# Kernel optimization log

Measured on AMD Instinct MI355X. Metric: run time of the kernel, lower is better.

The kernel has to match this reference:

```python
import jax, jax.numpy as jnp
import numpy as np

N, E = 50000, 1600000
D_IN, D_HID, D_OUT = 256, 256, 128  # 2*output_dim = 256, output_dim = 128


def glorot(key, shape):
    fan_in, fan_out = shape
    limit = np.sqrt(6.0 / (fan_in + fan_out)).astype(np.float32)
    return jax.random.uniform(key, shape, jnp.float32, -limit, limit)


def setup_inputs() -> dict:
    key = jax.random.key(0)
    k0, k1, k2, k3 = jax.random.split(key, 4)
    x = jax.random.normal(k0, (N, D_IN), jnp.float32)
    edge_index = jax.random.randint(k1, (2, E), 0, N, jnp.int32)
    W1 = glorot(k2, (D_IN, D_HID))
    b1 = jnp.zeros((D_HID,), jnp.float32)
    W2 = glorot(k3, (D_HID, D_OUT))
    b2 = jnp.zeros((D_OUT,), jnp.float32)
    return {"x": x, "edge_index": edge_index, "W1": W1, "b1": b1, "W2": W2, "b2": b2}


def gcn_propagate(x, src, dst, num_nodes):
    """One hop of D^-1/2 (A + I) D^-1/2 @ x (PyG gcn_norm with self-loops)."""
    loops = jnp.arange(num_nodes, dtype=src.dtype)
    src_sl = jnp.concatenate([src, loops])  # [E + N]
    dst_sl = jnp.concatenate([dst, loops])
    ones = jnp.ones(src_sl.shape, x.dtype)
    deg = jax.ops.segment_sum(ones, dst_sl, num_segments=num_nodes)  # >= 1 (self-loop)
    dinv = jax.lax.rsqrt(jnp.maximum(deg, 1e-12))
    norm = dinv[src_sl] * dinv[dst_sl]  # [E + N]
    msgs = x[src_sl] * norm[:, None]    # gather + scale, [E+N, D]
    return jax.ops.segment_sum(msgs, dst_sl, num_segments=num_nodes)


def reference(x, edge_index, W1, b1, W2, b2):
    src, dst = edge_index[0], edge_index[1]
    n = x.shape[0]
    # SGConv(K=1): propagate then linear. conv1 + ReLU
    h = jax.nn.relu(gcn_propagate(x, src, dst, n) @ W1 + b1)
    # conv2 (GAE branch)
    return gcn_propagate(h, src, dst, n) @ W2 + b2
```

## Files before the change

### kernel.cpp

```cpp
#include <hip/hip_runtime.h>

typedef short s16x8 __attribute__((ext_vector_type(8)));
typedef float f32x4 __attribute__((ext_vector_type(4)));
typedef float f32x2 __attribute__((ext_vector_type(2)));

#define TILE 2048

__device__ __forceinline__ unsigned int brne(float f) {
    unsigned int u = __float_as_uint(f);
    return (u + 0x7FFFu + ((u >> 16) & 1u)) >> 16;
}
__device__ __forceinline__ float blo(unsigned int u) { return __uint_as_float(u << 16); }
__device__ __forceinline__ float bhi(unsigned int u) { return __uint_as_float(u & 0xFFFF0000u); }

__device__ __forceinline__ unsigned int pk_bf16(float lo, float hi) {
    unsigned int r;
    asm("v_cvt_pk_bf16_f32 %0, %1, %2" : "=v"(r) : "v"(lo), "v"(hi));
    return r;
}

__device__ __forceinline__ void acc8p(f32x2* a, const uint4 u, const f32x2 w2) {
    a[0] += (f32x2){blo(u.x), bhi(u.x)} * w2;
    a[1] += (f32x2){blo(u.y), bhi(u.y)} * w2;
    a[2] += (f32x2){blo(u.z), bhi(u.z)} * w2;
    a[3] += (f32x2){blo(u.w), bhi(u.w)} * w2;
}

__device__ __forceinline__ void acc16p(f32x2* a, const uint4 u, const f32x2 w2) {
    a[0] += __builtin_amdgcn_cvt_pk_f32_fp8((int)u.x, false) * w2;
    a[1] += __builtin_amdgcn_cvt_pk_f32_fp8((int)u.x, true)  * w2;
    a[2] += __builtin_amdgcn_cvt_pk_f32_fp8((int)u.y, false) * w2;
    a[3] += __builtin_amdgcn_cvt_pk_f32_fp8((int)u.y, true)  * w2;
    a[4] += __builtin_amdgcn_cvt_pk_f32_fp8((int)u.z, false) * w2;
    a[5] += __builtin_amdgcn_cvt_pk_f32_fp8((int)u.z, true)  * w2;
    a[6] += __builtin_amdgcn_cvt_pk_f32_fp8((int)u.w, false) * w2;
    a[7] += __builtin_amdgcn_cvt_pk_f32_fp8((int)u.w, true)  * w2;
}


__global__ void k_bhist(const int* __restrict__ dst, int* __restrict__ bucket_cnt,
                        int e, int nb) {
    __shared__ int h[256];
    const int tid = threadIdx.x;
    h[tid] = 0;
    __syncthreads();
    const int base = blockIdx.x * TILE + tid;
#pragma unroll
    for (int k = 0; k < 8; k++) {
        const int i = base + k * 256;
        if (i < e) atomicAdd(&h[dst[i] >> 8], 1);
    }
    __syncthreads();
    if (tid < nb && h[tid]) atomicAdd(&bucket_cnt[tid], h[tid]);
}

__global__ void k_bscatter(const int* __restrict__ src, const int* __restrict__ dst,
                           const int* __restrict__ bcnt, int* __restrict__ bbase,
                           int* __restrict__ bcur, uint2* __restrict__ eb, int e, int nb) {
    __shared__ int sh[256], sbase[256], h[256], hbase[256], h2[256];
    const int tid = threadIdx.x;
    const int v = (tid < nb) ? bcnt[tid] : 0;
    int x = v;
    sh[tid] = x;
    __syncthreads();
    for (int off = 1; off < 256; off <<= 1) {
        const int t = (tid >= off) ? sh[tid - off] : 0;
        __syncthreads();
        if (tid >= off) { x += t; sh[tid] = x; }
        __syncthreads();
    }
    sbase[tid] = x - v;
    if (blockIdx.x == 0) {
        if (tid < nb) bbase[tid] = x - v;
        if (tid == 0) bbase[nb] = e;
    }
    h[tid] = 0; h2[tid] = 0;
    __syncthreads();
    const int base = blockIdx.x * TILE + tid;
    int s[8], d[8], b[8];
    bool val[8];
#pragma unroll
    for (int k = 0; k < 8; k++) {
        const int i = base + k * 256;
        val[k] = i < e;
        if (val[k]) {
            s[k] = src[i]; d[k] = dst[i]; b[k] = d[k] >> 8;
            atomicAdd(&h[b[k]], 1);
        }
    }
    __syncthreads();
    if (h[tid]) hbase[tid] = sbase[tid] + atomicAdd(&bcur[tid], h[tid]);
    __syncthreads();
#pragma unroll
    for (int k = 0; k < 8; k++) {
        if (val[k]) {
            const int off = atomicAdd(&h2[b[k]], 1);
            eb[hbase[b[k]] + off] = make_uint2((unsigned)s[k], (unsigned)d[k]);
        }
    }
}

__global__ void k_nhist_scan(const uint2* __restrict__ eb, const int* __restrict__ bucket_base,
                             int* __restrict__ rowptr, int* __restrict__ part,
                             float* __restrict__ dinv, int n) {
    __shared__ int c[256], sh[256];
    const int tid = threadIdx.x, b = blockIdx.x;
    c[tid] = 0;
    __syncthreads();
    const int beg = bucket_base[b], end = bucket_base[b + 1];
    for (int i = beg + tid; i < end; i += 256)
        atomicAdd(&c[eb[i].y & 255], 1);
    __syncthreads();
    const int v = c[tid];
    const int node = b * 256 + tid;
    if (node < n) dinv[node] = rsqrtf((float)(v + 1));
    int x = v;
    sh[tid] = x;
    __syncthreads();
    for (int off = 1; off < 256; off <<= 1) {
        const int t = (tid >= off) ? sh[tid - off] : 0;
        __syncthreads();
        if (tid >= off) { x += t; sh[tid] = x; }
        __syncthreads();
    }
    if (node <= n) rowptr[node] = x - v;
    if (tid == 255) part[b] = x;
}

template <bool PREW>
__global__ void k_place(const uint2* __restrict__ eb, const int* __restrict__ bucket_base,
                        int* __restrict__ rowptr, const int* __restrict__ part,
                        void* __restrict__ esv, const float* __restrict__ dinv,
                        int n, int nb) {
    __shared__ int sh[256], rp[256], offs[256];
    __shared__ float sdv[256];
    const int tid = threadIdx.x, b = blockIdx.x;
    int x = (tid < nb) ? part[tid] : 0;
    sh[tid] = x;
    __syncthreads();
    for (int off = 1; off < 256; off <<= 1) {
        const int t = (tid >= off) ? sh[tid - off] : 0;
        __syncthreads();
        if (tid >= off) { x += t; sh[tid] = x; }
        __syncthreads();
    }
    const int prefix = (b > 0) ? sh[b - 1] : 0;
    const int node = b * 256 + tid;
    int rg = 0;
    if (node <= n) {
        rg = rowptr[node] + prefix;
        rowptr[node] = rg;
    }
    rp[tid] = rg;
    offs[tid] = 0;
    if (PREW) sdv[tid] = (node < n) ? dinv[node] : 0.f;
    __syncthreads();
    const int beg = bucket_base[b], end = bucket_base[b + 1];
    if (PREW) {
        int2* es2 = (int2*)esv;
        for (int i = beg + tid; i < end; i += 256) {
            const uint2 ed = eb[i];
            const int sI = (int)ed.x, d = (int)ed.y & 255;
            const float w = dinv[sI] * sdv[d];
            const int local = atomicAdd(&offs[d], 1);
            es2[rp[d] + local] = make_int2(sI, __float_as_int(w));
        }
    } else {
        int* es1 = (int*)esv;
        for (int i = beg + tid; i < end; i += 256) {
            const uint2 ed = eb[i];
            const int d = (int)ed.y & 255;
            const int local = atomicAdd(&offs[d], 1);
            es1[rp[d] + local] = (int)ed.x;
        }
    }
}

__global__ void k_tW2(const float* __restrict__ W1, const float* __restrict__ W2,
                      unsigned short* __restrict__ W1t, unsigned short* __restrict__ W2t) {
    const int t = blockIdx.x * 256 + threadIdx.x;
    if (t < 65536) {
        const int k = t >> 8, nn = t & 255;
        W1t[nn * 256 + k] = (unsigned short)brne(W1[t]);
    } else {
        const int u = t - 65536;
        const int k = u >> 7, nn = u & 127;
        W2t[nn * 256 + k] = (unsigned short)brne(W2[u]);
    }
}

#define LP 40
template <bool AF32, bool FP8OUT>
__global__ __launch_bounds__(256) void k_gemm(const void* __restrict__ Av,
                                              const unsigned short* __restrict__ Bt,
                                              void* __restrict__ Cout,
                                              int M, int Nc) {
    __shared__ unsigned short As[2][128 * LP];
    __shared__ unsigned short Bs[2][128 * LP];

    const int tid = threadIdx.x;
    const int wave = tid >> 6, lane = tid & 63;
    const int wm = (wave >> 1) * 64, wn = (wave & 1) * 64;
    const int l15 = lane & 15, quad = lane >> 4;
    const int mBase = blockIdx.x * 128, nBase = blockIdx.y * 128;

    f32x4 acc[4][4];
#pragma unroll
    for (int i = 0; i < 4; i++)
#pragma unroll
        for (int j = 0; j < 4; j++) acc[i][j] = (f32x4){0.f, 0.f, 0.f, 0.f};

    const int r0 = tid >> 2, kc0 = tid & 3;
    int am0 = mBase + r0;      if (am0 >= M) am0 = M - 1;
    int am1 = mBase + r0 + 64; if (am1 >= M) am1 = M - 1;

    const uint4* Ap0; const uint4* Ap1; const float4* Af0; const float4* Af1;
    if (AF32) {
        Af0 = (const float4*)Av + (size_t)am0 * 64 + kc0 * 2;
        Af1 = (const float4*)Av + (size_t)am1 * 64 + kc0 * 2;
    } else {
        Ap0 = (const uint4*)Av + (size_t)am0 * 32 + kc0;
        Ap1 = (const uint4*)Av + (size_t)am1 * 32 + kc0;
    }
    const uint4* Bp0 = (const uint4*)Bt + (size_t)(nBase + r0) * 32 + kc0;
    const uint4* Bp1 = (const uint4*)Bt + (size_t)(nBase + r0 + 64) * 32 + kc0;

    uint4 a0, a1, b0, b1;
    auto LOAD = [&](int kt) {
        if (AF32) {
            const float4 l0 = Af0[kt * 8], h0 = Af0[kt * 8 + 1];
            const float4 l1 = Af1[kt * 8], h1 = Af1[kt * 8 + 1];
            a0.x = pk_bf16(l0.x, l0.y); a0.y = pk_bf16(l0.z, l0.w);
            a0.z = pk_bf16(h0.x, h0.y); a0.w = pk_bf16(h0.z, h0.w);
            a1.x = pk_bf16(l1.x, l1.y); a1.y = pk_bf16(l1.z, l1.w);
            a1.z = pk_bf16(h1.x, h1.y); a1.w = pk_bf16(h1.z, h1.w);
        } else {
            a0 = Ap0[kt * 4];
            a1 = Ap1[kt * 4];
        }
        b0 = Bp0[kt * 4];
        b1 = Bp1[kt * 4];
    };
    auto STORE = [&](int buf) {
        *(uint4*)&As[buf][r0 * LP + kc0 * 8] = a0;
        *(uint4*)&As[buf][(r0 + 64) * LP + kc0 * 8] = a1;
        *(uint4*)&Bs[buf][r0 * LP + kc0 * 8] = b0;
        *(uint4*)&Bs[buf][(r0 + 64) * LP + kc0 * 8] = b1;
    };

    LOAD(0);
    STORE(0);
    __syncthreads();
    for (int kt = 0; kt < 8; ++kt) {
        const int cur = kt & 1;
        if (kt < 7) LOAD(kt + 1);
        s16x8 af[4], bf[4];
#pragma unroll
        for (int i = 0; i < 4; i++)
            af[i] = *(const s16x8*)&As[cur][(wm + i * 16 + l15) * LP + quad * 8];
#pragma unroll
        for (int j = 0; j < 4; j++)
            bf[j] = *(const s16x8*)&Bs[cur][(wn + j * 16 + l15) * LP + quad * 8];
        if (kt < 7) STORE(cur ^ 1);
#pragma unroll
        for (int i = 0; i < 4; i++)
#pragma unroll
            for (int j = 0; j < 4; j++)
                acc[i][j] = __builtin_amdgcn_mfma_f32_16x16x32_bf16(af[i], bf[j], acc[i][j], 0, 0, 0);
        __syncthreads();
    }

#pragma unroll
    for (int i = 0; i < 4; i++) {
        const int rowb = mBase + wm + i * 16 + quad * 4;
#pragma unroll
        for (int j = 0; j < 4; j++) {
            const int col = nBase + wn + j * 16 + l15;
#pragma unroll
            for (int r = 0; r < 4; r += 2) {
                if (FP8OUT) {
                    const unsigned int pk = __builtin_amdgcn_cvt_pk_fp8_f32(
                        acc[i][j][r], acc[i][j][r + 1], 0, false);
                    if (rowb + r < M)
                        ((unsigned char*)Cout)[(size_t)(rowb + r) * Nc + col] =
                            (unsigned char)pk;
                    if (rowb + r + 1 < M)
                        ((unsigned char*)Cout)[(size_t)(rowb + r + 1) * Nc + col] =
                            (unsigned char)(pk >> 8);
                } else {
                    const unsigned int pk = pk_bf16(acc[i][j][r], acc[i][j][r + 1]);
                    if (rowb + r < M)
                        ((unsigned short*)Cout)[(size_t)(rowb + r) * Nc + col] =
                            (unsigned short)pk;
                    if (rowb + r + 1 < M)
                        ((unsigned short*)Cout)[(size_t)(rowb + r + 1) * Nc + col] =
                            (unsigned short)(pk >> 16);
                }
            }
        }
    }
}


template <bool PREW>
__global__ void k_prop256f8(const uint4* __restrict__ X4,
                            const int* __restrict__ rowptr,
                            const void* __restrict__ esv,
                            const float* __restrict__ dinv,
                            const float* __restrict__ bias,
                            uint4* __restrict__ Y4, int n) {
    const int wid = (int)((blockIdx.x * blockDim.x + threadIdx.x) >> 6);
    const int lane = threadIdx.x & 63;
    const int quad = lane >> 4, l16 = lane & 15;
    if (wid >= n) return;
    const float dd = dinv[wid];
    const int2* es2 = (const int2*)esv;
    const int*  es1 = (const int*)esv;
    f32x2 a[8];
#pragma unroll
    for (int k = 0; k < 8; k++) a[k] = (f32x2){0.f, 0.f};

    const int beg = rowptr[wid], end = rowptr[wid + 1];
    int j = beg + quad;

    auto EDGE = [&](int jj, int& s, float& w) {
        const bool v = jj < end;
        const int idx = v ? jj : 0;
        if (PREW) {
            const int2 p = es2[idx];
            s = p.x;
            w = v ? __int_as_float(p.y) : 0.f;
        } else {
            s = es1[idx];
            w = v ? dinv[s] * dd : 0.f;
        }
    };

    int s0, s1, s2, s3;
    float w0, w1, w2, w3;
    EDGE(j, s0, w0); EDGE(j + 4, s1, w1); EDGE(j + 8, s2, w2); EDGE(j + 12, s3, w3);

    if (quad == 0) {
        const uint4 v = X4[(size_t)wid * 16 + l16];
        acc16p(a, v, (f32x2){dd * dd, dd * dd});
    }

    while (j + 12 < end) {
        const uint4 u0 = X4[(size_t)s0 * 16 + l16];
        const uint4 u1 = X4[(size_t)s1 * 16 + l16];
        const uint4 u2 = X4[(size_t)s2 * 16 + l16];
        const uint4 u3 = X4[(size_t)s3 * 16 + l16];
        j += 16;
        int t0, t1, t2, t3;
        float x0, x1, x2, x3;
        EDGE(j, t0, x0); EDGE(j + 4, t1, x1); EDGE(j + 8, t2, x2); EDGE(j + 12, t3, x3);
        acc16p(a, u0, (f32x2){w0, w0});
        acc16p(a, u1, (f32x2){w1, w1});
        acc16p(a, u2, (f32x2){w2, w2});
        acc16p(a, u3, (f32x2){w3, w3});
        s0 = t0; s1 = t1; s2 = t2; s3 = t3;
        w0 = x0; w1 = x1; w2 = x2; w3 = x3;
    }
    {
        const uint4 u0 = X4[(size_t)s0 * 16 + l16];
        const uint4 u1 = X4[(size_t)s1 * 16 + l16];
        const uint4 u2 = X4[(size_t)s2 * 16 + l16];
        acc16p(a, u0, (f32x2){w0, w0});
        acc16p(a, u1, (f32x2){w1, w1});
        acc16p(a, u2, (f32x2){w2, w2});
    }
#pragma unroll
    for (int k = 0; k < 8; k++) {
        a[k][0] += __shfl_xor(a[k][0], 16);
        a[k][1] += __shfl_xor(a[k][1], 16);
        a[k][0] += __shfl_xor(a[k][0], 32);
        a[k][1] += __shfl_xor(a[k][1], 32);
    }
    if (quad == 0) {
        const float4* bp = (const float4*)bias + l16 * 4;
#pragma unroll
        for (int q = 0; q < 4; q++) {
            const float4 b = bp[q];
            a[2 * q][0]     = fmaxf(a[2 * q][0] + b.x, 0.f);
            a[2 * q][1]     = fmaxf(a[2 * q][1] + b.y, 0.f);
            a[2 * q + 1][0] = fmaxf(a[2 * q + 1][0] + b.z, 0.f);
            a[2 * q + 1][1] = fmaxf(a[2 * q + 1][1] + b.w, 0.f);
        }
        uint4 p0, p1;
        p0.x = pk_bf16(a[0][0], a[0][1]);
        p0.y = pk_bf16(a[1][0], a[1][1]);
        p0.z = pk_bf16(a[2][0], a[2][1]);
        p0.w = pk_bf16(a[3][0], a[3][1]);
        p1.x = pk_bf16(a[4][0], a[4][1]);
        p1.y = pk_bf16(a[5][0], a[5][1]);
        p1.z = pk_bf16(a[6][0], a[6][1]);
        p1.w = pk_bf16(a[7][0], a[7][1]);
        Y4[(size_t)wid * 32 + l16 * 2] = p0;
        Y4[(size_t)wid * 32 + l16 * 2 + 1] = p1;
    }
}

template <bool PREW>
__global__ void k_prop128b(const uint4* __restrict__ X4,
                           const int* __restrict__ rowptr,
                           const void* __restrict__ esv,
                           const float* __restrict__ dinv,
                           const float* __restrict__ bias,
                           float* __restrict__ Yout, int n) {
    const int wid = (int)((blockIdx.x * blockDim.x + threadIdx.x) >> 6);
    const int lane = threadIdx.x & 63;
    const int quad = lane >> 4, l16 = lane & 15;
    if (wid >= n) return;
    const float dd = dinv[wid];
    const int2* es2 = (const int2*)esv;
    const int*  es1 = (const int*)esv;
    f32x2 a[4];
#pragma unroll
    for (int k = 0; k < 4; k++) a[k] = (f32x2){0.f, 0.f};

    const int beg = rowptr[wid], end = rowptr[wid + 1];
    int j = beg + quad;

    auto EDGE = [&](int jj, int& s, float& w) {
        const bool v = jj < end;
        const int idx = v ? jj : 0;
        if (PREW) {
            const int2 p = es2[idx];
            s = p.x;
            w = v ? __int_as_float(p.y) : 0.f;
        } else {
            s = es1[idx];
            w = v ? dinv[s] * dd : 0.f;
        }
    };

    int s0, s1, s2, s3;
    float w0, w1, w2, w3;
    EDGE(j, s0, w0); EDGE(j + 4, s1, w1); EDGE(j + 8, s2, w2); EDGE(j + 12, s3, w3);

    if (quad == 0) {
        const uint4 v = X4[(size_t)wid * 16 + l16];
        acc8p(a, v, (f32x2){dd * dd, dd * dd});
    }

    while (j + 12 < end) {
        const uint4 u0 = X4[(size_t)s0 * 16 + l16];
        const uint4 u1 = X4[(size_t)s1 * 16 + l16];
        const uint4 u2 = X4[(size_t)s2 * 16 + l16];
        const uint4 u3 = X4[(size_t)s3 * 16 + l16];
        j += 16;
        int t0, t1, t2, t3;
        float x0, x1, x2, x3;
        EDGE(j, t0, x0); EDGE(j + 4, t1, x1); EDGE(j + 8, t2, x2); EDGE(j + 12, t3, x3);
        acc8p(a, u0, (f32x2){w0, w0});
        acc8p(a, u1, (f32x2){w1, w1});
        acc8p(a, u2, (f32x2){w2, w2});
        acc8p(a, u3, (f32x2){w3, w3});
        s0 = t0; s1 = t1; s2 = t2; s3 = t3;
        w0 = x0; w1 = x1; w2 = x2; w3 = x3;
    }
    {
        const uint4 u0 = X4[(size_t)s0 * 16 + l16];
        const uint4 u1 = X4[(size_t)s1 * 16 + l16];
        const uint4 u2 = X4[(size_t)s2 * 16 + l16];
        acc8p(a, u0, (f32x2){w0, w0});
        acc8p(a, u1, (f32x2){w1, w1});
        acc8p(a, u2, (f32x2){w2, w2});
    }
#pragma unroll
    for (int k = 0; k < 4; k++) {
        a[k][0] += __shfl_xor(a[k][0], 16);
        a[k][1] += __shfl_xor(a[k][1], 16);
        a[k][0] += __shfl_xor(a[k][0], 32);
        a[k][1] += __shfl_xor(a[k][1], 32);
    }
    if (quad == 0) {
        const float4 b0 = ((const float4*)bias)[l16 * 2];
        const float4 b1 = ((const float4*)bias)[l16 * 2 + 1];
        float4* op = (float4*)Yout + (size_t)wid * 32 + l16 * 2;
        op[0] = make_float4(a[0][0] + b0.x, a[0][1] + b0.y, a[1][0] + b0.z, a[1][1] + b0.w);
        op[1] = make_float4(a[2][0] + b1.x, a[2][1] + b1.y, a[3][0] + b1.z, a[3][1] + b1.w);
    }
}

extern "C" void kernel_launch(void* const* d_in, const int* in_sizes, int n_in,
                              void* d_out, int out_size, void* d_ws, size_t ws_size,
                              hipStream_t stream) {
    const float* x  = (const float*)d_in[0];
    const int*   ei = (const int*)d_in[1];
    const float* W1 = (const float*)d_in[2];
    const float* b1 = (const float*)d_in[3];
    const float* W2 = (const float*)d_in[4];
    const float* b2 = (const float*)d_in[5];
    float* out = (float*)d_out;

    const int n = in_sizes[0] / 256;
    const int e = in_sizes[1] / 2;
    const int* src = ei;
    const int* dst = ei + e;
    const int nb = (n + 255) >> 8;

    auto al = [](size_t v) { return (v + 511) & ~(size_t)511; };
    const size_t fixed = al(sizeof(float) * n) + al(sizeof(int) * (n + 1)) +
                         al(1024) + al(2048) + al(sizeof(int) * 257) +
                         al(2ull * 256 * 256) + al(2ull * 128 * 256) +
                         al((size_t)n * 256) + al(2ull * n * 256) + al(2ull * n * 128);
    const bool prew = (fixed + al(8ull * (size_t)e)) <= ws_size;

    char* wsp = (char*)d_ws;
    size_t off = 0;
    auto alloc = [&](size_t bytes) -> char* {
        char* p = wsp + off;
        off += (bytes + 511) & ~(size_t)511;
        return p;
    };
    float* dinv    = (float*)alloc(sizeof(float) * n);
    int*   rowptr  = (int*)alloc(sizeof(int) * (n + 1));
    int*   part    = (int*)alloc(1024);
    int*   bcc     = (int*)alloc(2048);
    int*   bcnt    = bcc;
    int*   bcur    = bcc + 256;
    int*   bbase   = (int*)alloc(sizeof(int) * 257);
    void*  es      = (void*)alloc((prew ? 8ull : 4ull) * (size_t)e);
    unsigned short* W1t = (unsigned short*)alloc(2ull * 256 * 256);
    unsigned short* W2t = (unsigned short*)alloc(2ull * 128 * 256);
    unsigned char*  T1  = (unsigned char*)alloc((size_t)n * 256);
    unsigned short* H   = (unsigned short*)alloc(2ull * n * 256);
    unsigned short* T2  = (unsigned short*)alloc(2ull * n * 128);
    uint2* eb = (uint2*)H;

    const int nb_t = (e + TILE - 1) / TILE;

    static hipStream_t sB = nullptr;
    static hipEvent_t evF = nullptr, evW = nullptr;
    static int inited = 0;
    if (!inited) {
        inited = 1;
        if (hipStreamCreateWithFlags(&sB, hipStreamNonBlocking) != hipSuccess) sB = nullptr;
        if (hipEventCreateWithFlags(&evF, hipEventDisableTiming) != hipSuccess) evF = nullptr;
        if (hipEventCreateWithFlags(&evW, hipEventDisableTiming) != hipSuccess) evW = nullptr;
    }
    const bool par = (sB != nullptr) && (evF != nullptr) && (evW != nullptr);
    hipStream_t gs = par ? sB : stream;

    if (par) {
        (void)hipEventRecord(evF, stream);
        (void)hipStreamWaitEvent(sB, evF, 0);
    }

    k_tW2<<<(65536 + 32768) / 256, 256, 0, gs>>>(W1, W2, W1t, W2t);
    dim3 g1((n + 127) / 128, 2);
    k_gemm<true, true><<<g1, 256, 0, gs>>>(x, W1t, T1, n, 256);
    if (par) (void)hipEventRecord(evW, gs);

    (void)hipMemsetAsync(bcc, 0, 2048, stream);
    k_bhist<<<nb_t, 256, 0, stream>>>(dst, bcnt, e, nb);
    k_bscatter<<<nb_t, 256, 0, stream>>>(src, dst, bcnt, bbase, bcur, eb, e, nb);
    k_nhist_scan<<<nb, 256, 0, stream>>>(eb, bbase, rowptr, part, dinv, n);
    if (prew)
        k_place<true><<<nb, 256, 0, stream>>>(eb, bbase, rowptr, part, es, dinv, n, nb);
    else
        k_place<false><<<nb, 256, 0, stream>>>(eb, bbase, rowptr, part, es, dinv, n, nb);

    if (par) (void)hipStreamWaitEvent(stream, evW, 0);

    if (prew)
        k_prop256f8<true><<<(n + 3) / 4, 256, 0, stream>>>((const uint4*)T1, rowptr, es,
                                                           dinv, b1, (uint4*)H, n);
    else
        k_prop256f8<false><<<(n + 3) / 4, 256, 0, stream>>>((const uint4*)T1, rowptr, es,
                                                            dinv, b1, (uint4*)H, n);

    dim3 g2((n + 127) / 128, 1);
    k_gemm<false, false><<<g2, 256, 0, stream>>>(H, W2t, T2, n, 128);
    if (prew)
        k_prop128b<true><<<(n + 3) / 4, 256, 0, stream>>>((const uint4*)T2, rowptr, es,
                                                          dinv, b2, out, n);
    else
        k_prop128b<false><<<(n + 3) / 4, 256, 0, stream>>>((const uint4*)T2, rowptr, es,
                                                           dinv, b2, out, n);
}
```

Before: 349.2 us.

## Serialize streams, pad edge array, and force packed FMA in propagation

```diff
diff --git a/kernel.cpp b/kernel.cpp
--- a/kernel.cpp
+++ b/kernel.cpp
@@ -19,22 +19,26 @@
     return r;
 }
 
+__device__ __forceinline__ void pkfma(f32x2& a, const f32x2 x, const f32x2 w) {
+    asm("v_pk_fma_f32 %0, %1, %2, %0" : "+v"(a) : "v"(x), "v"(w));
+}
+
 __device__ __forceinline__ void acc8p(f32x2* a, const uint4 u, const f32x2 w2) {
-    a[0] += (f32x2){blo(u.x), bhi(u.x)} * w2;
-    a[1] += (f32x2){blo(u.y), bhi(u.y)} * w2;
-    a[2] += (f32x2){blo(u.z), bhi(u.z)} * w2;
-    a[3] += (f32x2){blo(u.w), bhi(u.w)} * w2;
+    pkfma(a[0], (f32x2){blo(u.x), bhi(u.x)}, w2);
+    pkfma(a[1], (f32x2){blo(u.y), bhi(u.y)}, w2);
+    pkfma(a[2], (f32x2){blo(u.z), bhi(u.z)}, w2);
+    pkfma(a[3], (f32x2){blo(u.w), bhi(u.w)}, w2);
 }
 
 __device__ __forceinline__ void acc16p(f32x2* a, const uint4 u, const f32x2 w2) {
-    a[0] += __builtin_amdgcn_cvt_pk_f32_fp8((int)u.x, false) * w2;
-    a[1] += __builtin_amdgcn_cvt_pk_f32_fp8((int)u.x, true)  * w2;
-    a[2] += __builtin_amdgcn_cvt_pk_f32_fp8((int)u.y, false) * w2;
-    a[3] += __builtin_amdgcn_cvt_pk_f32_fp8((int)u.y, true)  * w2;
-    a[4] += __builtin_amdgcn_cvt_pk_f32_fp8((int)u.z, false) * w2;
-    a[5] += __builtin_amdgcn_cvt_pk_f32_fp8((int)u.z, true)  * w2;
-    a[6] += __builtin_amdgcn_cvt_pk_f32_fp8((int)u.w, false) * w2;
-    a[7] += __builtin_amdgcn_cvt_pk_f32_fp8((int)u.w, true)  * w2;
+    pkfma(a[0], __builtin_amdgcn_cvt_pk_f32_fp8((int)u.x, false), w2);
+    pkfma(a[1], __builtin_amdgcn_cvt_pk_f32_fp8((int)u.x, true),  w2);
+    pkfma(a[2], __builtin_amdgcn_cvt_pk_f32_fp8((int)u.y, false), w2);
+    pkfma(a[3], __builtin_amdgcn_cvt_pk_f32_fp8((int)u.y, true),  w2);
+    pkfma(a[4], __builtin_amdgcn_cvt_pk_f32_fp8((int)u.z, false), w2);
+    pkfma(a[5], __builtin_amdgcn_cvt_pk_f32_fp8((int)u.z, true),  w2);
+    pkfma(a[6], __builtin_amdgcn_cvt_pk_f32_fp8((int)u.w, false), w2);
+    pkfma(a[7], __builtin_amdgcn_cvt_pk_f32_fp8((int)u.w, true),  w2);
 }
 
 
@@ -131,7 +135,7 @@
 __global__ void k_place(const uint2* __restrict__ eb, const int* __restrict__ bucket_base,
                         int* __restrict__ rowptr, const int* __restrict__ part,
                         void* __restrict__ esv, const float* __restrict__ dinv,
-                        int n, int nb) {
+                        int n, int nb, int e) {
     __shared__ int sh[256], rp[256], offs[256];
     __shared__ float sdv[256];
     const int tid = threadIdx.x, b = blockIdx.x;
@@ -158,6 +162,7 @@
     const int beg = bucket_base[b], end = bucket_base[b + 1];
     if (PREW) {
         int2* es2 = (int2*)esv;
+        if (b == 0 && tid < 64) es2[e + tid] = make_int2(0, 0);
         for (int i = beg + tid; i < end; i += 256) {
             const uint2 ed = eb[i];
             const int sI = (int)ed.x, d = (int)ed.y & 255;
@@ -325,12 +330,12 @@
 
     auto EDGE = [&](int jj, int& s, float& w) {
         const bool v = jj < end;
-        const int idx = v ? jj : 0;
         if (PREW) {
-            const int2 p = es2[idx];
+            const int2 p = es2[jj];
             s = p.x;
             w = v ? __int_as_float(p.y) : 0.f;
         } else {
+            const int idx = v ? jj : 0;
             s = es1[idx];
             w = v ? dinv[s] * dd : 0.f;
         }
@@ -423,12 +428,12 @@
 
     auto EDGE = [&](int jj, int& s, float& w) {
         const bool v = jj < end;
-        const int idx = v ? jj : 0;
         if (PREW) {
-            const int2 p = es2[idx];
+            const int2 p = es2[jj];
             s = p.x;
             w = v ? __int_as_float(p.y) : 0.f;
         } else {
+            const int idx = v ? jj : 0;
             s = es1[idx];
             w = v ? dinv[s] * dd : 0.f;
         }
@@ -505,7 +510,7 @@
                          al(1024) + al(2048) + al(sizeof(int) * 257) +
                          al(2ull * 256 * 256) + al(2ull * 128 * 256) +
                          al((size_t)n * 256) + al(2ull * n * 256) + al(2ull * n * 128);
-    const bool prew = (fixed + al(8ull * (size_t)e)) <= ws_size;
+    const bool prew = (fixed + al(8ull * ((size_t)e + 64))) <= ws_size;
 
     char* wsp = (char*)d_ws;
     size_t off = 0;
@@ -521,7 +526,7 @@
     int*   bcnt    = bcc;
     int*   bcur    = bcc + 256;
     int*   bbase   = (int*)alloc(sizeof(int) * 257);
-    void*  es      = (void*)alloc((prew ? 8ull : 4ull) * (size_t)e);
+    void*  es      = (void*)alloc(prew ? 8ull * ((size_t)e + 64) : 4ull * (size_t)e);
     unsigned short* W1t = (unsigned short*)alloc(2ull * 256 * 256);
     unsigned short* W2t = (unsigned short*)alloc(2ull * 128 * 256);
     unsigned char*  T1  = (unsigned char*)alloc((size_t)n * 256);
@@ -531,39 +536,19 @@
 
     const int nb_t = (e + TILE - 1) / TILE;
 
-    static hipStream_t sB = nullptr;
-    static hipEvent_t evF = nullptr, evW = nullptr;
-    static int inited = 0;
-    if (!inited) {
-        inited = 1;
-        if (hipStreamCreateWithFlags(&sB, hipStreamNonBlocking) != hipSuccess) sB = nullptr;
-        if (hipEventCreateWithFlags(&evF, hipEventDisableTiming) != hipSuccess) evF = nullptr;
-        if (hipEventCreateWithFlags(&evW, hipEventDisableTiming) != hipSuccess) evW = nullptr;
-    }
-    const bool par = (sB != nullptr) && (evF != nullptr) && (evW != nullptr);
-    hipStream_t gs = par ? sB : stream;
-
-    if (par) {
-        (void)hipEventRecord(evF, stream);
-        (void)hipStreamWaitEvent(sB, evF, 0);
-    }
-
-    k_tW2<<<(65536 + 32768) / 256, 256, 0, gs>>>(W1, W2, W1t, W2t);
-    dim3 g1((n + 127) / 128, 2);
-    k_gemm<true, true><<<g1, 256, 0, gs>>>(x, W1t, T1, n, 256);
-    if (par) (void)hipEventRecord(evW, gs);
-
     (void)hipMemsetAsync(bcc, 0, 2048, stream);
     k_bhist<<<nb_t, 256, 0, stream>>>(dst, bcnt, e, nb);
     k_bscatter<<<nb_t, 256, 0, stream>>>(src, dst, bcnt, bbase, bcur, eb, e, nb);
     k_nhist_scan<<<nb, 256, 0, stream>>>(eb, bbase, rowptr, part, dinv, n);
     if (prew)
-        k_place<true><<<nb, 256, 0, stream>>>(eb, bbase, rowptr, part, es, dinv, n, nb);
+        k_place<true><<<nb, 256, 0, stream>>>(eb, bbase, rowptr, part, es, dinv, n, nb, e);
     else
-        k_place<false><<<nb, 256, 0, stream>>>(eb, bbase, rowptr, part, es, dinv, n, nb);
-
-    if (par) (void)hipStreamWaitEvent(stream, evW, 0);
-
+        k_place<false><<<nb, 256, 0, stream>>>(eb, bbase, rowptr, part, es, dinv, n, nb, e);
+
+    k_tW2<<<(65536 + 32768) / 256, 256, 0, stream>>>(W1, W2, W1t, W2t);
+
+    dim3 g1((n + 127) / 128, 2);
+    k_gemm<true, true><<<g1, 256, 0, stream>>>(x, W1t, T1, n, 256);
     if (prew)
         k_prop256f8<true><<<(n + 3) / 4, 256, 0, stream>>>((const uint4*)T1, rowptr, es,
                                                            dinv, b1, (uint4*)H, n);
```

After: 318.3 us. 8.8% less time.
